# Kernel optimization log

Hardware: AMD Instinct MI355X
Metric: run time of the kernel (lower is better)

The kernel has to match this reference:

```python
import jax, jax.numpy as jnp
import numpy as np

EDGE = 32          # ImageEdge
KPOOL = 16         # pool_kernel_size = ImageEdge // 2
POOLED = 17        # 1 + ImageEdge - pool_kernel_size
NH = 12            # num_attention_heads
HD = 64            # head_dim
HID = 768          # hidden_size
SR = 2             # ScaleRatio


def setup_inputs() -> dict:
    key = jax.random.key(0)
    k1, k2, k3, k4 = jax.random.split(key, 4)
    B, Q = 8, 2048
    return {
        "image_hidden_states": jax.random.normal(k1, (B, EDGE * EDGE, HID), jnp.float32),
        "text_hidden_states": jax.random.normal(k2, (B, Q, HID), jnp.float32),
        "W_in": jax.random.normal(k3, (HID, HID), jnp.float32) * 0.02,   # input_proj (no bias)
        "W_up": jax.random.normal(k4, (HD, HD * SR * SR), jnp.float32) * 0.02,  # up_proj (no bias)
    }


def reference(image_hidden_states, text_hidden_states, W_in, W_up):
    img, txt = image_hidden_states, text_hidden_states
    B, S, HSZ = img.shape            # S = 1024
    Q = txt.shape[1]
    residual = img

    # cross-attention: text queries attend over image keys
    q = txt.reshape(B, Q, NH, HD).transpose(0, 2, 1, 3)   # [B,H,Q,D]
    k = img.reshape(B, S, NH, HD).transpose(0, 2, 1, 3)   # [B,H,S,D]
    attn = jnp.einsum('bhqd,bhkd->bhqk', q, k) / jnp.sqrt(jnp.float32(HD))
    attn = jax.nn.softmax(attn, axis=-1)                  # [B,H,Q,S]
    # dropout is identity in eval mode

    # pooled attention saliency map
    image_attn = attn.sum(axis=2).reshape(B, NH, EDGE, EDGE)
    pooled = jax.lax.reduce_window(
        image_attn, 0.0, jax.lax.add,
        window_dimensions=(1, 1, KPOOL, KPOOL),
        window_strides=(1, 1, 1, 1), padding='VALID') / (KPOOL * KPOOL)   # [B,H,17,17]
    idx = jnp.argmax(pooled.reshape(B, NH, -1), axis=-1)  # [B,H]
    row = (idx // POOLED).reshape(-1)
    col = (idx % POOLED).reshape(-1)

    # gather the argmax-selected 16x16 region per (batch, head)
    states = img.reshape(B, S, NH, HD).transpose(0, 2, 1, 3)
    states = states.reshape(B * NH, EDGE, EDGE, HD)
    slice_one = lambda s, r, c: jax.lax.dynamic_slice(s, (r, c, 0), (KPOOL, KPOOL, HD))
    region = jax.vmap(slice_one)(states, row, col)        # [B*H,16,16,D]

    # pixel-shuffle upsample back to 32x32
    up = region @ W_up                                    # [B*H,16,16,4*D]
    up = up.reshape(B, NH, KPOOL, KPOOL, SR, SR, HD)
    up = up.transpose(0, 1, 2, 4, 3, 5, 6)                # [B,H,16,2,16,2,D]
    up = up.reshape(B, NH, EDGE * EDGE, HD)
    out = up.transpose(0, 2, 1, 3).reshape(B, EDGE * EDGE, HSZ)

    # dense proj + gelu + residual
    out = jax.nn.gelu(out @ W_in, approximate=False)
    return residual + out
```

## Files before the change

kernel.cpp:

```cpp
#include <hip/hip_runtime.h>
#include <cstdint>
#include <cstddef>

#define BB    8
#define NH    12
#define BH    96
#define SS    1024
#define QQ    2048
#define DD    64
#define HID   768
#define EDGE  32
#define KPOOL 16
#define POOLED 17

typedef short bf16x8 __attribute__((ext_vector_type(8)));
typedef _Float16 f16x8 __attribute__((ext_vector_type(8)));
typedef float f32x4  __attribute__((ext_vector_type(4)));

#define MFMA16B(a, b, c) __builtin_amdgcn_mfma_f32_16x16x32_bf16((a), (b), (c), 0, 0, 0)
#define MFMA16H(a, b, c) __builtin_amdgcn_mfma_f32_16x16x32_f16((a), (b), (c), 0, 0, 0)

#define QSCALE 0.18033688011112042f

#if __has_builtin(__builtin_amdgcn_exp2f)
#define EXP2(x) __builtin_amdgcn_exp2f(x)
#else
#define EXP2(x) exp2f(x)
#endif

__device__ __forceinline__ short f2bf(float x) {
    unsigned u = __builtin_bit_cast(unsigned, x);
    u = u + 0x7fffu + ((u >> 16) & 1u);
    return (short)(u >> 16);
}
__device__ __forceinline__ f16x8 ash(bf16x8 v) {
    return __builtin_bit_cast(f16x8, v);
}

__device__ __forceinline__ size_t fragaddr(int row, int k) {
    return ((size_t)(row >> 4) * 24 + (k >> 5)) * 512 + ((k >> 3) & 3) * 128
         + (row & 15) * 8 + (k & 7);
}

__device__ __forceinline__ size_t partaddr(size_t j) {
    return (j >> 9) * 1024 + 512 + (j & 511);
}


__global__ __launch_bounds__(256) void k_castq(const float* __restrict__ txt,
                                               short* __restrict__ Qs) {
    int i = blockIdx.x * 256 + threadIdx.x;
    int quad = i & 3, kh = (i >> 2) & 1;
    int row = i >> 3;
    int c = row & 15, g = row >> 4;
    int q = row & 2047, bh = row >> 11;
    int b = bh / NH, h = bh - b * NH;
    const float* sp = txt + ((size_t)b * QQ + q) * HID + h * DD + kh * 32 + quad * 8;
    bf16x8 vh;
#pragma unroll
    for (int j = 0; j < 8; j++) {
        _Float16 hi = (_Float16)(sp[j] * QSCALE);
        vh[j] = __builtin_bit_cast(short, hi);
    }
    *(bf16x8*)(Qs + (size_t)g * 2048 + kh * 512 + quad * 128 + c * 8) = vh;
}

__global__ __launch_bounds__(256) void k_castk(const float* __restrict__ img,
                                               short* __restrict__ Ks) {
    int i = blockIdx.x * 256 + threadIdx.x;
    int quad = i & 3, kh = (i >> 2) & 1;
    int row = i >> 3;
    int c = row & 15, g = row >> 4;
    int s = row & 1023, bh = row >> 10;
    int b = bh / NH, h = bh - b * NH;
    const float* sp = img + ((size_t)b * SS + s) * HID + h * DD + kh * 32 + quad * 8;
    bf16x8 vh;
#pragma unroll
    for (int j = 0; j < 8; j++) {
        _Float16 hi = (_Float16)sp[j];
        vh[j] = __builtin_bit_cast(short, hi);
    }
    *(bf16x8*)(Ks + (size_t)g * 2048 + kh * 512 + quad * 128 + c * 8) = vh;
}

__global__ __launch_bounds__(256) void k_castw(const float* __restrict__ W,
                                               const float* __restrict__ Wup,
                                               short* __restrict__ Wt,
                                               short* __restrict__ Wupb) {
    if (blockIdx.x == 144) {
        for (int i = threadIdx.x; i < 16384; i += 256) {
            int k = i >> 8, n = i & 255;
            int addr = (n >> 4) * 1024 + (k >> 5) * 512 + ((k >> 3) & 3) * 128
                     + (n & 15) * 8 + (k & 7);
            Wupb[addr] = f2bf(Wup[k * 256 + n]);
        }
        return;
    }
    __shared__ float T[64][65];
    int bx = blockIdx.x % 12, by = blockIdx.x / 12;
    for (int i = threadIdx.x; i < 4096; i += 256) {
        int r = i >> 6, cc = i & 63;
        T[r][cc] = W[(size_t)(by * 64 + r) * HID + bx * 64 + cc];
    }
    __syncthreads();
    for (int i = threadIdx.x; i < 4096; i += 256) {
        int r = i >> 6, cc = i & 63;
        int n = bx * 64 + r, k = by * 64 + cc;
        Wt[fragaddr(n, k)] = f2bf(T[cc][r]);
    }
}

__global__ __launch_bounds__(512) void k_fused(const short* __restrict__ Qs,
                                               const short* __restrict__ Ks,
                                               float* __restrict__ Part) {
    __shared__ short Kt[2][8192];
    __shared__ float iacc[2][1024];
    __shared__ float Lred[2][4][16];

    int m = blockIdx.x;
    int bh = ((m >> 9) << 3) | (m & 7);
    int qb = (m >> 3) & 63;
    int tid = threadIdx.x;
    int w = tid >> 6, lane = tid & 63;
    int qi = w >> 2, si = w & 3;
    int quad = lane >> 4, c = lane & 15;

    const short* ap = Qs + ((size_t)bh * 128 + qb * 2 + qi) * 2048 + lane * 8;
    f16x8 a0 = ash(*(const bf16x8*)(ap));
    f16x8 a1 = ash(*(const bf16x8*)(ap + 512));

    const short* kbase = Ks + (size_t)bh * SS * 128;
    size_t s0 = (size_t)(tid >> 7) * 2048 + (size_t)(tid & 127) * 8;
    int i1 = tid + 512;
    size_t s1 = (size_t)(i1 >> 7) * 2048 + (size_t)(i1 & 127) * 8;

    f32x4 pt[16];
    bf16x8 st0 = *(const bf16x8*)(kbase + s0);
    bf16x8 st1 = *(const bf16x8*)(kbase + s1);

#pragma unroll
    for (int cc = 0; cc < 8; cc++) {
        int buf = cc & 1;
        *(bf16x8*)(&Kt[buf][tid * 8]) = st0;
        *(bf16x8*)(&Kt[buf][(tid + 512) * 8]) = st1;
        if (cc + 1 < 8) {
            st0 = *(const bf16x8*)(kbase + (size_t)(cc + 1) * 16384 + s0);
            st1 = *(const bf16x8*)(kbase + (size_t)(cc + 1) * 16384 + s1);
        }
        __syncthreads();
#pragma unroll
        for (int h = 0; h < 2; h++) {
            const short* kp = &Kt[buf][(si + h * 4) * 1024 + lane * 8];
            f16x8 kb0 = ash(*(const bf16x8*)(kp));
            f16x8 kb1 = ash(*(const bf16x8*)(kp + 512));
            f32x4 acc = (f32x4){0.f, 0.f, 0.f, 0.f};
            acc = MFMA16H(a0, kb0, acc);
            acc = MFMA16H(a1, kb1, acc);
#pragma unroll
            for (int r = 0; r < 4; r++) pt[cc * 2 + h][r] = EXP2(acc[r]);
        }
    }

    float rl[4];
#pragma unroll
    for (int r = 0; r < 4; r++) {
        float v = 0.f;
#pragma unroll
        for (int cc = 0; cc < 16; cc++) v += pt[cc][r];
        v += __shfl_xor(v, 1);
        v += __shfl_xor(v, 2);
        v += __shfl_xor(v, 4);
        v += __shfl_xor(v, 8);
        if (c == 0) Lred[qi][si][quad * 4 + r] = v;
    }
    __syncthreads();
#pragma unroll
    for (int r = 0; r < 4; r++)
        rl[r] = __builtin_amdgcn_rcpf(
            Lred[qi][0][quad * 4 + r] + Lred[qi][1][quad * 4 + r] +
            Lred[qi][2][quad * 4 + r] + Lred[qi][3][quad * 4 + r]);

#pragma unroll
    for (int cc = 0; cc < 8; cc++) {
#pragma unroll
        for (int h = 0; h < 2; h++) {
            float v = pt[cc * 2 + h][0] * rl[0] + pt[cc * 2 + h][1] * rl[1]
                    + pt[cc * 2 + h][2] * rl[2] + pt[cc * 2 + h][3] * rl[3];
            v += __shfl_xor(v, 16);
            v += __shfl_xor(v, 32);
            if (lane < 16) iacc[qi][cc * 128 + (si + h * 4) * 16 + lane] = v;
        }
    }
    __syncthreads();
    for (int i = tid; i < 1024; i += 512) {
        size_t j = ((size_t)(bh * 64 + qb)) * 1024 + i;
        Part[partaddr(j)] = iacc[0][i] + iacc[1][i];
    }
}

__global__ __launch_bounds__(256) void k_reduce(const float* __restrict__ Part,
                                                float* __restrict__ iattn) {
    int bh = blockIdx.x >> 2, quarter = blockIdx.x & 3;
    int s = quarter * 256 + threadIdx.x;
    float v = 0.f;
#pragma unroll 8
    for (int qb = 0; qb < 64; qb++) {
        size_t j = ((size_t)(bh * 64 + qb)) * 1024 + s;
        v += Part[partaddr(j)];
    }
    iattn[(size_t)bh * SS + s] = v;
}

__global__ __launch_bounds__(256, 2) void k_up(const float* __restrict__ img,
                                               const float* __restrict__ iattn,
                                               const short* __restrict__ Wupb,
                                               short* __restrict__ Xb) {
    __shared__ short Reg[16384];
    float* F = (float*)Reg;
    float* Apool = F;
    float* Vp = F + 1024;
    float* bvp = F + 1568;
    int*   bip = (int*)(F + 1824);

    int bh = blockIdx.x >> 2, nq = blockIdx.x & 3;
    int b = bh / NH, h = bh - b * NH;
    int tid = threadIdx.x;
    int w = tid >> 6, lane = tid & 63;
    int quad = lane >> 4, c = lane & 15;

    for (int i = tid; i < 1024; i += 256) Apool[i] = iattn[(size_t)bh * SS + i];
    __syncthreads();
    for (int i = tid; i < POOLED * EDGE; i += 256) {
        int r = i >> 5, cc = i & 31;
        float s = 0.f;
#pragma unroll
        for (int k = 0; k < KPOOL; k++) s += Apool[(r + k) * EDGE + cc];
        Vp[i] = s;
    }
    __syncthreads();
    float best = -1e30f;
    int bidx = 1 << 30;
    for (int i = tid; i < POOLED * POOLED; i += 256) {
        int r = i / POOLED, cc = i - r * POOLED;
        float s = 0.f;
#pragma unroll
        for (int k = 0; k < KPOOL; k++) s += Vp[r * EDGE + cc + k];
        if (s > best || (s == best && i < bidx)) { best = s; bidx = i; }
    }
    bvp[tid] = best;
    bip[tid] = bidx;
    __syncthreads();
    for (int off = 128; off; off >>= 1) {
        if (tid < off) {
            float ov = bvp[tid + off];
            int oi = bip[tid + off];
            if (ov > bvp[tid] || (ov == bvp[tid] && oi < bip[tid])) {
                bvp[tid] = ov;
                bip[tid] = oi;
            }
        }
        __syncthreads();
    }
    int widx = bip[0];
    __syncthreads();
    int r0 = widx / POOLED, c0 = widx - r0 * POOLED;

    for (int p = tid; p < 2048; p += 256) {
        int pos = p >> 3, sub = p & 7;
        int gi = r0 + (pos >> 4), gj = c0 + (pos & 15);
        const float* sp = img + ((size_t)b * SS + gi * EDGE + gj) * HID + h * DD + sub * 8;
        bf16x8 v;
#pragma unroll
        for (int j = 0; j < 8; j++) v[j] = f2bf(sp[j]);
        *(bf16x8*)(&Reg[(pos >> 4) * 1024 + (sub >> 2) * 512 + (sub & 3) * 128 + (pos & 15) * 8]) = v;
    }
    __syncthreads();

    bf16x8 bu[4][2];
#pragma unroll
    for (int u = 0; u < 4; u++) {
#pragma unroll
        for (int kh = 0; kh < 2; kh++)
            bu[u][kh] = *(const bf16x8*)(Wupb + (nq * 4 + u) * 1024 + kh * 512 + lane * 8);
    }

#pragma unroll
    for (int t = 0; t < 4; t++) {
        int g = w * 4 + t;
        bf16x8 a0 = *(const bf16x8*)(&Reg[g * 1024 + lane * 8]);
        bf16x8 a1 = *(const bf16x8*)(&Reg[g * 1024 + 512 + lane * 8]);
#pragma unroll
        for (int u = 0; u < 4; u++) {
            f32x4 acc = (f32x4){0.f, 0.f, 0.f, 0.f};
            acc = MFMA16B(a0, bu[u][0], acc);
            acc = MFMA16B(a1, bu[u][1], acc);
#pragma unroll
            for (int r = 0; r < 4; r++) {
                int pos = g * 16 + quad * 4 + r;
                int oc = nq * 64 + u * 16 + c;
                int i16 = pos >> 4, j16 = pos & 15;
                int a = oc >> 7, bbit = (oc >> 6) & 1, dp = oc & 63;
                int p2 = (2 * i16 + a) * EDGE + (2 * j16 + bbit);
                int row = b * SS + p2, kdim = h * DD + dp;
                Xb[fragaddr(row, kdim)] = f2bf(acc[r]);
            }
        }
    }
}

__global__ __launch_bounds__(256) void k_out(const short* __restrict__ Xb,
                                             const short* __restrict__ Wt,
                                             const float* __restrict__ img,
                                             float* __restrict__ out) {
    __shared__ short At[2][4096];
    __shared__ short Bt[2][2048];
    int mblk = blockIdx.x & 63, nblk = blockIdx.x >> 6;
    int tid = threadIdx.x;
    int w = tid >> 6, lane = tid & 63;
    int quad = lane >> 4, c = lane & 15;
    int gm0 = mblk * 8, gn0 = nblk * 4;
    int m0 = mblk * 128, n0 = nblk * 64;

    int ua1 = tid + 256;
    const short* srcA0 = Xb + ((size_t)(gm0 + (tid >> 6)) * 24) * 512 + (tid & 63) * 8;
    const short* srcA1 = Xb + ((size_t)(gm0 + (ua1 >> 6)) * 24) * 512 + (ua1 & 63) * 8;
    const short* srcB  = Wt + ((size_t)(gn0 + (tid >> 6)) * 24) * 512 + (tid & 63) * 8;

    f32x4 acc[2][4];
#pragma unroll
    for (int t = 0; t < 2; t++)
#pragma unroll
        for (int u = 0; u < 4; u++) acc[t][u] = (f32x4){0.f, 0.f, 0.f, 0.f};

    bf16x8 sa0 = *(const bf16x8*)(srcA0);
    bf16x8 sa1 = *(const bf16x8*)(srcA1);
    bf16x8 sb  = *(const bf16x8*)(srcB);

    for (int kk = 0; kk < 24; kk++) {
        int buf = kk & 1;
        *(bf16x8*)(&At[buf][tid * 8]) = sa0;
        *(bf16x8*)(&At[buf][ua1 * 8]) = sa1;
        *(bf16x8*)(&Bt[buf][tid * 8]) = sb;
        if (kk + 1 < 24) {
            sa0 = *(const bf16x8*)(srcA0 + (kk + 1) * 512);
            sa1 = *(const bf16x8*)(srcA1 + (kk + 1) * 512);
            sb  = *(const bf16x8*)(srcB  + (kk + 1) * 512);
        }
        __syncthreads();
        bf16x8 a0 = *(const bf16x8*)(&At[buf][(2 * w + 0) * 512 + lane * 8]);
        bf16x8 a1 = *(const bf16x8*)(&At[buf][(2 * w + 1) * 512 + lane * 8]);
        bf16x8 b0 = *(const bf16x8*)(&Bt[buf][0 * 512 + lane * 8]);
        bf16x8 b1 = *(const bf16x8*)(&Bt[buf][1 * 512 + lane * 8]);
        bf16x8 b2 = *(const bf16x8*)(&Bt[buf][2 * 512 + lane * 8]);
        bf16x8 b3 = *(const bf16x8*)(&Bt[buf][3 * 512 + lane * 8]);
        acc[0][0] = MFMA16B(a0, b0, acc[0][0]);
        acc[0][1] = MFMA16B(a0, b1, acc[0][1]);
        acc[0][2] = MFMA16B(a0, b2, acc[0][2]);
        acc[0][3] = MFMA16B(a0, b3, acc[0][3]);
        acc[1][0] = MFMA16B(a1, b0, acc[1][0]);
        acc[1][1] = MFMA16B(a1, b1, acc[1][1]);
        acc[1][2] = MFMA16B(a1, b2, acc[1][2]);
        acc[1][3] = MFMA16B(a1, b3, acc[1][3]);
    }

#pragma unroll
    for (int t = 0; t < 2; t++) {
#pragma unroll
        for (int u = 0; u < 4; u++) {
#pragma unroll
            for (int r = 0; r < 4; r++) {
                int row = m0 + w * 32 + t * 16 + quad * 4 + r;
                int col = n0 + u * 16 + c;
                float x = acc[t][u][r];
                float g = 0.5f * x * (1.f + erff(x * 0.70710678118654752f));
                size_t o = (size_t)row * HID + col;
                out[o] = img[o] + g;
            }
        }
    }
}

extern "C" void kernel_launch(void* const* d_in, const int* in_sizes, int n_in,
                              void* d_out, int out_size, void* d_ws, size_t ws_size,
                              hipStream_t stream) {
    const float* img = (const float*)d_in[0];
    const float* txt = (const float*)d_in[1];
    const float* Win = (const float*)d_in[2];
    const float* Wup = (const float*)d_in[3];
    float* out = (float*)d_out;

    char* w = (char*)d_ws;
    short* Qs    = (short*)(w);
    short* Ks    = (short*)(w + 50331648);
    short* Wt    = (short*)(w + 75497472);
    float* iattn = (float*)(w + 77463552);
    short* Wupb  = (short*)(w + 77856768);
    float* Part  = (float*)(w);
    short* Xb    = (short*)(w);

    k_castq<<<dim3(6144), dim3(256), 0, stream>>>(txt, Qs);
    k_castk<<<dim3(3072), dim3(256), 0, stream>>>(img, Ks);
    k_castw<<<dim3(145), dim3(256), 0, stream>>>(Win, Wup, Wt, Wupb);
    k_fused<<<dim3(6144), dim3(512), 0, stream>>>(Qs, Ks, Part);
    k_reduce<<<dim3(384), dim3(256), 0, stream>>>(Part, iattn);
    k_up<<<dim3(384), dim3(256), 0, stream>>>(img, iattn, Wupb, Xb);
    k_out<<<dim3(768), dim3(256), 0, stream>>>(Xb, Wt, img, out);
}
```

Baseline: 261.4 us.

## Fuse query cast into attention kernel and replace partial reduce with atomics

New measurement: 262.3 us. About the same (+0.4%).

```diff
diff --git a/kernel.cpp b/kernel.cpp
--- a/kernel.cpp
+++ b/kernel.cpp
@@ -42,28 +42,6 @@
          + (row & 15) * 8 + (k & 7);
 }
 
-__device__ __forceinline__ size_t partaddr(size_t j) {
-    return (j >> 9) * 1024 + 512 + (j & 511);
-}
-
-
-__global__ __launch_bounds__(256) void k_castq(const float* __restrict__ txt,
-                                               short* __restrict__ Qs) {
-    int i = blockIdx.x * 256 + threadIdx.x;
-    int quad = i & 3, kh = (i >> 2) & 1;
-    int row = i >> 3;
-    int c = row & 15, g = row >> 4;
-    int q = row & 2047, bh = row >> 11;
-    int b = bh / NH, h = bh - b * NH;
-    const float* sp = txt + ((size_t)b * QQ + q) * HID + h * DD + kh * 32 + quad * 8;
-    bf16x8 vh;
-#pragma unroll
-    for (int j = 0; j < 8; j++) {
-        _Float16 hi = (_Float16)(sp[j] * QSCALE);
-        vh[j] = __builtin_bit_cast(short, hi);
-    }
-    *(bf16x8*)(Qs + (size_t)g * 2048 + kh * 512 + quad * 128 + c * 8) = vh;
-}
 
 __global__ __launch_bounds__(256) void k_castk(const float* __restrict__ img,
                                                short* __restrict__ Ks) {
@@ -110,9 +88,9 @@
     }
 }
 
-__global__ __launch_bounds__(512) void k_fused(const short* __restrict__ Qs,
+__global__ __launch_bounds__(512) void k_fused(const float* __restrict__ txt,
                                                const short* __restrict__ Ks,
-                                               float* __restrict__ Part) {
+                                               float* __restrict__ iattn) {
     __shared__ short Kt[2][8192];
     __shared__ float iacc[2][1024];
     __shared__ float Lred[2][4][16];
@@ -124,10 +102,16 @@
     int w = tid >> 6, lane = tid & 63;
     int qi = w >> 2, si = w & 3;
     int quad = lane >> 4, c = lane & 15;
-
-    const short* ap = Qs + ((size_t)bh * 128 + qb * 2 + qi) * 2048 + lane * 8;
-    f16x8 a0 = ash(*(const bf16x8*)(ap));
-    f16x8 a1 = ash(*(const bf16x8*)(ap + 512));
+    int b = bh / NH, h = bh - b * NH;
+
+    int q = qb * 32 + qi * 16 + c;
+    const float* sp = txt + ((size_t)b * QQ + q) * HID + h * DD + quad * 8;
+    f16x8 a0, a1;
+#pragma unroll
+    for (int j = 0; j < 8; j++) {
+        a0[j] = (_Float16)(sp[j] * QSCALE);
+        a1[j] = (_Float16)(sp[32 + j] * QSCALE);
+    }
 
     const short* kbase = Ks + (size_t)bh * SS * 128;
     size_t s0 = (size_t)(tid >> 7) * 2048 + (size_t)(tid & 127) * 8;
@@ -149,15 +133,15 @@
         }
         __syncthreads();
 #pragma unroll
-        for (int h = 0; h < 2; h++) {
-            const short* kp = &Kt[buf][(si + h * 4) * 1024 + lane * 8];
+        for (int hh = 0; hh < 2; hh++) {
+            const short* kp = &Kt[buf][(si + hh * 4) * 1024 + lane * 8];
             f16x8 kb0 = ash(*(const bf16x8*)(kp));
             f16x8 kb1 = ash(*(const bf16x8*)(kp + 512));
             f32x4 acc = (f32x4){0.f, 0.f, 0.f, 0.f};
             acc = MFMA16H(a0, kb0, acc);
             acc = MFMA16H(a1, kb1, acc);
 #pragma unroll
-            for (int r = 0; r < 4; r++) pt[cc * 2 + h][r] = EXP2(acc[r]);
+            for (int r = 0; r < 4; r++) pt[cc * 2 + hh][r] = EXP2(acc[r]);
         }
     }
 
@@ -183,32 +167,17 @@
 #pragma unroll
     for (int cc = 0; cc < 8; cc++) {
 #pragma unroll
-        for (int h = 0; h < 2; h++) {
-            float v = pt[cc * 2 + h][0] * rl[0] + pt[cc * 2 + h][1] * rl[1]
-                    + pt[cc * 2 + h][2] * rl[2] + pt[cc * 2 + h][3] * rl[3];
+        for (int hh = 0; hh < 2; hh++) {
+            float v = pt[cc * 2 + hh][0] * rl[0] + pt[cc * 2 + hh][1] * rl[1]
+                    + pt[cc * 2 + hh][2] * rl[2] + pt[cc * 2 + hh][3] * rl[3];
             v += __shfl_xor(v, 16);
             v += __shfl_xor(v, 32);
-            if (lane < 16) iacc[qi][cc * 128 + (si + h * 4) * 16 + lane] = v;
-        }
-    }
-    __syncthreads();
-    for (int i = tid; i < 1024; i += 512) {
-        size_t j = ((size_t)(bh * 64 + qb)) * 1024 + i;
-        Part[partaddr(j)] = iacc[0][i] + iacc[1][i];
-    }
-}
-
-__global__ __launch_bounds__(256) void k_reduce(const float* __restrict__ Part,
-                                                float* __restrict__ iattn) {
-    int bh = blockIdx.x >> 2, quarter = blockIdx.x & 3;
-    int s = quarter * 256 + threadIdx.x;
-    float v = 0.f;
-#pragma unroll 8
-    for (int qb = 0; qb < 64; qb++) {
-        size_t j = ((size_t)(bh * 64 + qb)) * 1024 + s;
-        v += Part[partaddr(j)];
-    }
-    iattn[(size_t)bh * SS + s] = v;
+            if (lane < 16) iacc[qi][cc * 128 + (si + hh * 4) * 16 + lane] = v;
+        }
+    }
+    __syncthreads();
+    for (int i = tid; i < 1024; i += 512)
+        atomicAdd(&iattn[(size_t)bh * SS + i], iacc[0][i] + iacc[1][i]);
 }
 
 __global__ __launch_bounds__(256, 2) void k_up(const float* __restrict__ img,
@@ -390,19 +359,16 @@
     float* out = (float*)d_out;
 
     char* w = (char*)d_ws;
-    short* Qs    = (short*)(w);
     short* Ks    = (short*)(w + 50331648);
     short* Wt    = (short*)(w + 75497472);
     float* iattn = (float*)(w + 77463552);
     short* Wupb  = (short*)(w + 77856768);
-    float* Part  = (float*)(w);
     short* Xb    = (short*)(w);
 
-    k_castq<<<dim3(6144), dim3(256), 0, stream>>>(txt, Qs);
     k_castk<<<dim3(3072), dim3(256), 0, stream>>>(img, Ks);
     k_castw<<<dim3(145), dim3(256), 0, stream>>>(Win, Wup, Wt, Wupb);
-    k_fused<<<dim3(6144), dim3(512), 0, stream>>>(Qs, Ks, Part);
-    k_reduce<<<dim3(384), dim3(256), 0, stream>>>(Part, iattn);
+    hipMemsetAsync(iattn, 0, (size_t)BH * SS * sizeof(float), stream);
+    k_fused<<<dim3(6144), dim3(512), 0, stream>>>(txt, Ks, iattn);
     k_up<<<dim3(384), dim3(256), 0, stream>>>(img, iattn, Wupb, Xb);
     k_out<<<dim3(768), dim3(256), 0, stream>>>(Xb, Wt, img, out);
 }
```
